# Kernel optimization log

Hardware: AMD Instinct MI355X
Metric: run time of the kernel (lower is better)

Reference implementation:

```python
import jax, jax.numpy as jnp
import numpy as np

N = 100000      # nodes
E = 1600000     # edges (avg degree 16)
ND = 64         # node feature dim (fiber degree-0 channels)
ED = 32         # edge feature dim
L = 3           # number of edge_update layers (num_layers - 1)
IN = ED + 2 * ND  # concat dim = 160
EPS = 1e-5
NEG_SLOPE = 0.01  # torch LeakyReLU default


def setup_inputs() -> dict:
    key = jax.random.key(0)
    ks = jax.random.split(key, 6)
    node_feat = jax.random.normal(ks[0], (N, ND), jnp.float32)
    edge_w = jax.random.normal(ks[1], (E, ED), jnp.float32)
    edge_i = jax.random.randint(ks[2], (E,), 0, N, jnp.int32)
    edge_j = jax.random.randint(ks[3], (E,), 0, N, jnp.int32)
    ln_g = jnp.ones((L, IN), jnp.float32)
    ln_b = jnp.zeros((L, IN), jnp.float32)
    w1 = jax.random.normal(ks[4], (L, IN, ED), jnp.float32) / np.sqrt(IN).astype(np.float32)
    b1 = jnp.zeros((L, ED), jnp.float32)
    w2 = jax.random.normal(ks[5], (L, ED, ED), jnp.float32) / np.sqrt(ED).astype(np.float32)
    b2 = jnp.zeros((L, ED), jnp.float32)
    return {"node_feat": node_feat, "edge_w": edge_w, "ln_g": ln_g, "ln_b": ln_b,
            "w1": w1, "b1": b1, "w2": w2, "b2": b2,
            "edge_i": edge_i, "edge_j": edge_j}


def _edge_update(nf, e, g, b, W1, B1, W2, B2, i, j):
    # gather per-edge endpoint features, concat with edge feature: [E, IN]
    x = jnp.concatenate([nf[i], nf[j], e], axis=-1)
    # LayerNorm over last dim
    mu = jnp.mean(x, axis=-1, keepdims=True)
    var = jnp.var(x, axis=-1, keepdims=True)
    x = (x - mu) * jax.lax.rsqrt(var + EPS) * g + b
    # Linear -> LeakyReLU -> Linear
    x = x @ W1 + B1
    x = jnp.where(x > 0, x, NEG_SLOPE * x)
    x = x @ W2 + B2
    return e + x  # residual edge update


def reference(node_feat, edge_w, ln_g, ln_b, w1, b1, w2, b2, edge_i, edge_j):
    e = edge_w
    for l in range(ln_g.shape[0]):  # small fixed layer count
        e = _edge_update(node_feat, e, ln_g[l], ln_b[l], w1[l], b1[l], w2[l], b2[l], edge_i, edge_j)
    return e
```

## Files before the change

### kernel.cpp

```cpp
#include <hip/hip_runtime.h>

#define EE     1600000
#define NN     100000
#define NDIM   64
#define EDIM   32
#define NLAYER 3
#define INDIM  160
#define TPB    256
#define EPT    2
#define EPB    (TPB*EPT)

static_assert(EE % EPB == 0, "grid must divide evenly");

__global__ __launch_bounds__(TPB) void node_precompute(
  const float* __restrict__ nf,  const float* __restrict__ lng,
  const float* __restrict__ lnb, const float* __restrict__ w1,
  const float* __restrict__ b1,
  float* __restrict__ P, float* __restrict__ nstat, float* __restrict__ cvec)
{
  __shared__ float sW[NLAYER*128*EDIM];
  __shared__ float sG[NLAYER*128];
  const int tid = threadIdx.x;

  #pragma unroll
  for (int it = 0; it < 12; ++it){
    const int c = tid + it*TPB;
    const int l = c >> 10, rem = c & 1023;
    const int d = rem >> 3, ks = (rem & 7) * 4;
    float4 v = *(const float4*)(w1 + (size_t)l*INDIM*EDIM + d*EDIM + ks);
    float* dst = &sW[l*128*EDIM + d*EDIM + ks];
    dst[0]=v.x; dst[1]=v.y; dst[2]=v.z; dst[3]=v.w;
  }
  if (tid < 96){
    const int l = tid >> 5, ks = (tid & 31) * 4;
    float4 v = *(const float4*)(lng + l*INDIM + ks);
    float* dst = &sG[l*128 + ks];
    dst[0]=v.x; dst[1]=v.y; dst[2]=v.z; dst[3]=v.w;
  }
  __syncthreads();

  if (blockIdx.x == 0 && tid < 96){
    const int l = tid >> 5, k = tid & 31;
    const float* wl = w1 + (size_t)l*INDIM*EDIM;
    float c2 = 0.f, c1 = b1[l*EDIM + k];
    for (int d = 0; d < INDIM; ++d){
      const float w = wl[d*EDIM + k];
      c2 = fmaf(lng[l*INDIM + d], w, c2);
      c1 = fmaf(lnb[l*INDIM + d], w, c1);
    }
    cvec[l*EDIM + k]      = c2;
    cvec[96 + l*EDIM + k] = c1;
  }

  const int n = blockIdx.x*TPB + tid;
  if (n >= NN) return;
  const float4* px = (const float4*)(nf + (size_t)n * NDIM);

  {
    float s = 0.f, q = 0.f;
    #pragma unroll 1
    for (int c = 0; c < 16; ++c){
      float4 v = px[c];
      s += v.x + v.y + v.z + v.w;
      q = fmaf(v.x,v.x,q); q = fmaf(v.y,v.y,q);
      q = fmaf(v.z,v.z,q); q = fmaf(v.w,v.w,q);
    }
    nstat[2*n] = s; nstat[2*n+1] = q;
  }

  #pragma unroll 1
  for (int lp = 0; lp < NLAYER*2; ++lp){
    const int l = lp >> 1, part = lp & 1;
    float acc[EDIM];
    #pragma unroll
    for (int k = 0; k < EDIM; ++k) acc[k] = 0.f;
    const float* wbl = &sW[(l*128 + part*64) * EDIM];
    const float* gbl = &sG[l*128 + part*64];
    #pragma unroll 1
    for (int c = 0; c < 16; ++c){
      float4 xv = px[c];
      const float xs[4] = {xv.x, xv.y, xv.z, xv.w};
      const int d0 = 4*c;
      #pragma unroll
      for (int u = 0; u < 4; ++u){
        const float xd = xs[u] * gbl[d0 + u];
        const float4* row = (const float4*)&wbl[(size_t)(d0+u)*EDIM];
        #pragma unroll
        for (int q8 = 0; q8 < 8; ++q8){
          float4 w = row[q8];
          acc[4*q8+0] = fmaf(xd, w.x, acc[4*q8+0]);
          acc[4*q8+1] = fmaf(xd, w.y, acc[4*q8+1]);
          acc[4*q8+2] = fmaf(xd, w.z, acc[4*q8+2]);
          acc[4*q8+3] = fmaf(xd, w.w, acc[4*q8+3]);
        }
      }
    }
    float* dst = P + ((size_t)l*NN + n)*64 + part*EDIM;
    #pragma unroll
    for (int q8 = 0; q8 < 8; ++q8)
      ((float4*)dst)[q8] = make_float4(acc[4*q8+0], acc[4*q8+1], acc[4*q8+2], acc[4*q8+3]);
  }
}

__global__ __launch_bounds__(TPB, 2) void edge_mlp_pre(
  const float* __restrict__ ew, const float* __restrict__ lng,
  const float* __restrict__ w1, const float* __restrict__ w2,
  const float* __restrict__ b2,
  const int* __restrict__ ei, const int* __restrict__ ej,
  const float* __restrict__ P, const float* __restrict__ nstat,
  const float* __restrict__ cvec, float* __restrict__ out)
{
  __shared__ float sW1E[NLAYER*EDIM*EDIM];
  __shared__ float sW2 [NLAYER*EDIM*EDIM];
  __shared__ float sGE [NLAYER*EDIM];
  __shared__ float sC2 [NLAYER*EDIM], sC1b[NLAYER*EDIM], sB2v[NLAYER*EDIM];

  const int tid = threadIdx.x;
  #pragma unroll
  for (int it = 0; it < 3; ++it){
    const int c = tid + it*TPB;
    const int l = c >> 8, rem = c & 255;
    const int d = rem >> 3, ks = (rem & 7) * 4;
    float4 v = *(const float4*)(w1 + (size_t)l*INDIM*EDIM + (size_t)(128+d)*EDIM + ks);
    float* dst = &sW1E[l*EDIM*EDIM + d*EDIM + ks];
    dst[0]=v.x; dst[1]=v.y; dst[2]=v.z; dst[3]=v.w;
  }
  #pragma unroll
  for (int it = 0; it < 3; ++it){
    const int c = tid + it*TPB;
    float4 v = ((const float4*)w2)[c];
    float* dst = &sW2[4*c];
    dst[0]=v.x; dst[1]=v.y; dst[2]=v.z; dst[3]=v.w;
  }
  if (tid < 96){
    sGE [tid] = lng[(tid>>5)*INDIM + 128 + (tid&31)];
    sB2v[tid] = b2[tid];
    sC2 [tid] = cvec[tid];
    sC1b[tid] = cvec[96 + tid];
  }
  __syncthreads();

  const int id0 = blockIdx.x * EPB + tid;
  const int id1 = id0 + TPB;
  const int i0 = ei[id0], j0 = ej[id0];
  const int i1 = ei[id1], j1 = ej[id1];

  const float2 sti0 = *(const float2*)(nstat + 2*(size_t)i0);
  const float2 stj0 = *(const float2*)(nstat + 2*(size_t)j0);
  const float2 sti1 = *(const float2*)(nstat + 2*(size_t)i1);
  const float2 stj1 = *(const float2*)(nstat + 2*(size_t)j1);
  const float sn0 = sti0.x + stj0.x, qn0 = sti0.y + stj0.y;
  const float sn1 = sti1.x + stj1.x, qn1 = sti1.y + stj1.y;

  float e0[EDIM], e1[EDIM];
  {
    const float4* a = (const float4*)(ew + (size_t)id0 * EDIM);
    const float4* b = (const float4*)(ew + (size_t)id1 * EDIM);
    #pragma unroll
    for (int c = 0; c < 8; ++c){
      float4 v = a[c];
      e0[4*c+0]=v.x; e0[4*c+1]=v.y; e0[4*c+2]=v.z; e0[4*c+3]=v.w;
      float4 u = b[c];
      e1[4*c+0]=u.x; e1[4*c+1]=u.y; e1[4*c+2]=u.z; e1[4*c+3]=u.w;
    }
  }

  #pragma unroll 1
  for (int l = 0; l < NLAYER; ++l){
    const float* Pl = P + (size_t)l * NN * 64;
    const float4* a0v = (const float4*)(Pl + (size_t)i0*64);
    const float4* b0v = (const float4*)(Pl + (size_t)j0*64 + EDIM);
    const float4* a1v = (const float4*)(Pl + (size_t)i1*64);
    const float4* b1v = (const float4*)(Pl + (size_t)j1*64 + EDIM);

    float S0[EDIM], S1[EDIM];
    #pragma unroll
    for (int c = 0; c < 8; ++c){
      float4 u = a0v[c], v = b0v[c];
      S0[4*c+0]=u.x+v.x; S0[4*c+1]=u.y+v.y; S0[4*c+2]=u.z+v.z; S0[4*c+3]=u.w+v.w;
      float4 p = a1v[c], r = b1v[c];
      S1[4*c+0]=p.x+r.x; S1[4*c+1]=p.y+r.y; S1[4*c+2]=p.z+r.z; S1[4*c+3]=p.w+r.w;
    }

    float se0=0.f, qe0=0.f, se1=0.f, qe1=0.f;
    #pragma unroll
    for (int d = 0; d < EDIM; ++d){
      se0 += e0[d]; qe0 = fmaf(e0[d], e0[d], qe0);
      se1 += e1[d]; qe1 = fmaf(e1[d], e1[d], qe1);
    }
    const float mu0 = (sn0 + se0) * (1.f/INDIM);
    const float va0 = fmaxf(fmaf(-mu0, mu0, (qn0 + qe0) * (1.f/INDIM)), 0.f);
    const float rs0 = rsqrtf(va0 + 1e-5f);
    const float nm0 = -mu0 * rs0;
    const float mu1 = (sn1 + se1) * (1.f/INDIM);
    const float va1 = fmaxf(fmaf(-mu1, mu1, (qn1 + qe1) * (1.f/INDIM)), 0.f);
    const float rs1 = rsqrtf(va1 + 1e-5f);
    const float nm1 = -mu1 * rs1;

    const float* wE = &sW1E[l*EDIM*EDIM];
    const float* gE = &sGE[l*EDIM];
    #pragma unroll
    for (int d = 0; d < EDIM; ++d){
      const float xd0 = gE[d]*e0[d], xd1 = gE[d]*e1[d];
      const float4* row = (const float4*)&wE[d*EDIM];
      #pragma unroll
      for (int q = 0; q < 8; ++q){
        float4 w = row[q];
        S0[4*q+0]=fmaf(xd0,w.x,S0[4*q+0]); S1[4*q+0]=fmaf(xd1,w.x,S1[4*q+0]);
        S0[4*q+1]=fmaf(xd0,w.y,S0[4*q+1]); S1[4*q+1]=fmaf(xd1,w.y,S1[4*q+1]);
        S0[4*q+2]=fmaf(xd0,w.z,S0[4*q+2]); S1[4*q+2]=fmaf(xd1,w.z,S1[4*q+2]);
        S0[4*q+3]=fmaf(xd0,w.w,S0[4*q+3]); S1[4*q+3]=fmaf(xd1,w.w,S1[4*q+3]);
      }
    }

    const float* c2  = &sC2 [l*EDIM];
    const float* c1b = &sC1b[l*EDIM];
    const float* bb2 = &sB2v[l*EDIM];
    #pragma unroll
    for (int k = 0; k < EDIM; ++k){
      float a = fmaf(rs0, S0[k], fmaf(nm0, c2[k], c1b[k]));
      S0[k] = fmaxf(a, 0.01f*a);
      float b = fmaf(rs1, S1[k], fmaf(nm1, c2[k], c1b[k]));
      S1[k] = fmaxf(b, 0.01f*b);
    }
    #pragma unroll
    for (int k = 0; k < EDIM; ++k){ e0[k] += bb2[k]; e1[k] += bb2[k]; }

    const float* w2l = &sW2[l*EDIM*EDIM];
    #pragma unroll
    for (int d = 0; d < EDIM; ++d){
      const float a = S0[d], b = S1[d];
      const float4* row = (const float4*)&w2l[d*EDIM];
      #pragma unroll
      for (int q = 0; q < 8; ++q){
        float4 w = row[q];
        e0[4*q+0]=fmaf(a,w.x,e0[4*q+0]); e1[4*q+0]=fmaf(b,w.x,e1[4*q+0]);
        e0[4*q+1]=fmaf(a,w.y,e0[4*q+1]); e1[4*q+1]=fmaf(b,w.y,e1[4*q+1]);
        e0[4*q+2]=fmaf(a,w.z,e0[4*q+2]); e1[4*q+2]=fmaf(b,w.z,e1[4*q+2]);
        e0[4*q+3]=fmaf(a,w.w,e0[4*q+3]); e1[4*q+3]=fmaf(b,w.w,e1[4*q+3]);
      }
    }
  }

  float4* o0 = (float4*)(out + (size_t)id0 * EDIM);
  float4* o1 = (float4*)(out + (size_t)id1 * EDIM);
  #pragma unroll
  for (int c = 0; c < 8; ++c){
    o0[c] = make_float4(e0[4*c+0], e0[4*c+1], e0[4*c+2], e0[4*c+3]);
    o1[c] = make_float4(e1[4*c+0], e1[4*c+1], e1[4*c+2], e1[4*c+3]);
  }
}

__global__ __launch_bounds__(TPB, 2) void edge_mlp_fused(
  const float* __restrict__ nf,  const float* __restrict__ ew,
  const float* __restrict__ lng, const float* __restrict__ lnb,
  const float* __restrict__ w1,  const float* __restrict__ b1,
  const float* __restrict__ w2,  const float* __restrict__ b2,
  const int* __restrict__ ei, const int* __restrict__ ej,
  float* __restrict__ out)
{
  __shared__ float sW1[INDIM*EDIM];
  __shared__ float sW2[EDIM*EDIM];
  __shared__ float sC2[EDIM], sC1b[EDIM], sB2[EDIM];

  const int tid = threadIdx.x;
  const int id0 = blockIdx.x * EPB + tid;
  const int id1 = id0 + TPB;

  const float4* pi0 = (const float4*)(nf + (size_t)ei[id0] * NDIM);
  const float4* pj0 = (const float4*)(nf + (size_t)ej[id0] * NDIM);
  const float4* pi1 = (const float4*)(nf + (size_t)ei[id1] * NDIM);
  const float4* pj1 = (const float4*)(nf + (size_t)ej[id1] * NDIM);

  float e0[EDIM], e1[EDIM];
  {
    const float4* a = (const float4*)(ew + (size_t)id0 * EDIM);
    const float4* b = (const float4*)(ew + (size_t)id1 * EDIM);
    #pragma unroll
    for (int c = 0; c < 8; ++c){
      float4 v = a[c];
      e0[4*c+0]=v.x; e0[4*c+1]=v.y; e0[4*c+2]=v.z; e0[4*c+3]=v.w;
      float4 u = b[c];
      e1[4*c+0]=u.x; e1[4*c+1]=u.y; e1[4*c+2]=u.z; e1[4*c+3]=u.w;
    }
  }

  #pragma unroll 1
  for (int l = 0; l < NLAYER; ++l){
    __syncthreads();
    const float* w1l = w1 + (size_t)l * INDIM * EDIM;

    #pragma unroll
    for (int it = 0; it < 5; ++it){
      const int c = tid + it * TPB;
      const int d = c >> 3, ks = (c & 7) * 4;
      float4 v = *(const float4*)(w1l + d * EDIM + ks);
      const float g = lng[l * INDIM + d];
      sW1[d*EDIM+ks+0] = g*v.x; sW1[d*EDIM+ks+1] = g*v.y;
      sW1[d*EDIM+ks+2] = g*v.z; sW1[d*EDIM+ks+3] = g*v.w;
    }
    {
      const int d = tid >> 3, ks = (tid & 7) * 4;
      float4 v = *(const float4*)(w2 + (size_t)l*EDIM*EDIM + d*EDIM + ks);
      sW2[d*EDIM+ks+0] = v.x; sW2[d*EDIM+ks+1] = v.y;
      sW2[d*EDIM+ks+2] = v.z; sW2[d*EDIM+ks+3] = v.w;
    }
    if (tid < EDIM){
      float c1 = b1[l*EDIM + tid];
      for (int d = 0; d < INDIM; ++d)
        c1 = fmaf(lnb[l*INDIM + d], w1l[d*EDIM + tid], c1);
      sC1b[tid] = c1;
      sB2[tid]  = b2[l*EDIM + tid];
    }
    __syncthreads();
    if (tid < EDIM){
      float s = 0.f;
      for (int d = 0; d < INDIM; ++d) s += sW1[d*EDIM + tid];
      sC2[tid] = s;
    }
    __syncthreads();

    float S0[EDIM], S1[EDIM];
    #pragma unroll
    for (int k = 0; k < EDIM; ++k){ S0[k] = 0.f; S1[k] = 0.f; }
    float sum0 = 0.f, sq0 = 0.f, sum1 = 0.f, sq1 = 0.f;

    auto dot_row = [&](float xv0, float xv1, const float4* row){
      sum0 += xv0; sq0 = fmaf(xv0, xv0, sq0);
      sum1 += xv1; sq1 = fmaf(xv1, xv1, sq1);
      #pragma unroll
      for (int q = 0; q < 8; ++q){
        float4 w = row[q];
        S0[4*q+0] = fmaf(xv0, w.x, S0[4*q+0]); S1[4*q+0] = fmaf(xv1, w.x, S1[4*q+0]);
        S0[4*q+1] = fmaf(xv0, w.y, S0[4*q+1]); S1[4*q+1] = fmaf(xv1, w.y, S1[4*q+1]);
        S0[4*q+2] = fmaf(xv0, w.z, S0[4*q+2]); S1[4*q+2] = fmaf(xv1, w.z, S1[4*q+2]);
        S0[4*q+3] = fmaf(xv0, w.w, S0[4*q+3]); S1[4*q+3] = fmaf(xv1, w.w, S1[4*q+3]);
      }
    };

    #pragma unroll 1
    for (int c = 0; c < 32; ++c){
      const float4 x0 = (c < 16) ? pi0[c] : pj0[c - 16];
      const float4 x1 = (c < 16) ? pi1[c] : pj1[c - 16];
      const float4* wr = (const float4*)&sW1[c * 4 * EDIM];
      dot_row(x0.x, x1.x, wr + 0);
      dot_row(x0.y, x1.y, wr + 8);
      dot_row(x0.z, x1.z, wr + 16);
      dot_row(x0.w, x1.w, wr + 24);
    }
    #pragma unroll
    for (int d = 0; d < EDIM; ++d){
      const float4* row = (const float4*)&sW1[(2*NDIM + d) * EDIM];
      dot_row(e0[d], e1[d], row);
    }

    const float mu0 = sum0 * (1.f/INDIM);
    const float va0 = fmaxf(fmaf(-mu0, mu0, sq0 * (1.f/INDIM)), 0.f);
    const float rs0 = rsqrtf(va0 + 1e-5f);
    const float nm0 = -mu0 * rs0;
    const float mu1 = sum1 * (1.f/INDIM);
    const float va1 = fmaxf(fmaf(-mu1, mu1, sq1 * (1.f/INDIM)), 0.f);
    const float rs1 = rsqrtf(va1 + 1e-5f);
    const float nm1 = -mu1 * rs1;

    float h0[EDIM], h1v[EDIM];
    #pragma unroll
    for (int k = 0; k < EDIM; ++k){
      float a = fmaf(rs0, S0[k], fmaf(nm0, sC2[k], sC1b[k]));
      h0[k]  = fmaxf(a, 0.01f * a);
      float b = fmaf(rs1, S1[k], fmaf(nm1, sC2[k], sC1b[k]));
      h1v[k] = fmaxf(b, 0.01f * b);
    }
    #pragma unroll
    for (int k = 0; k < EDIM; ++k){ e0[k] += sB2[k]; e1[k] += sB2[k]; }
    #pragma unroll
    for (int d = 0; d < EDIM; ++d){
      const float a = h0[d], b = h1v[d];
      const float4* row = (const float4*)&sW2[d * EDIM];
      #pragma unroll
      for (int q = 0; q < 8; ++q){
        float4 w = row[q];
        e0[4*q+0] = fmaf(a, w.x, e0[4*q+0]); e1[4*q+0] = fmaf(b, w.x, e1[4*q+0]);
        e0[4*q+1] = fmaf(a, w.y, e0[4*q+1]); e1[4*q+1] = fmaf(b, w.y, e1[4*q+1]);
        e0[4*q+2] = fmaf(a, w.z, e0[4*q+2]); e1[4*q+2] = fmaf(b, w.z, e1[4*q+2]);
        e0[4*q+3] = fmaf(a, w.w, e0[4*q+3]); e1[4*q+3] = fmaf(b, w.w, e1[4*q+3]);
      }
    }
  }

  float4* o0 = (float4*)(out + (size_t)id0 * EDIM);
  float4* o1 = (float4*)(out + (size_t)id1 * EDIM);
  #pragma unroll
  for (int c = 0; c < 8; ++c){
    o0[c] = make_float4(e0[4*c+0], e0[4*c+1], e0[4*c+2], e0[4*c+3]);
    o1[c] = make_float4(e1[4*c+0], e1[4*c+1], e1[4*c+2], e1[4*c+3]);
  }
}

extern "C" void kernel_launch(void* const* d_in, const int* in_sizes, int n_in,
                              void* d_out, int out_size, void* d_ws, size_t ws_size,
                              hipStream_t stream)
{
  const float* nf  = (const float*)d_in[0];
  const float* ew  = (const float*)d_in[1];
  const float* lng = (const float*)d_in[2];
  const float* lnb = (const float*)d_in[3];
  const float* w1  = (const float*)d_in[4];
  const float* b1  = (const float*)d_in[5];
  const float* w2  = (const float*)d_in[6];
  const float* b2  = (const float*)d_in[7];
  const int*   ei  = (const int*)d_in[8];
  const int*   ej  = (const int*)d_in[9];
  float* out = (float*)d_out;

  const size_t PBYTES = (size_t)NLAYER * NN * 64 * sizeof(float);
  const size_t SBYTES = (size_t)NN * 2 * sizeof(float);
  const size_t CBYTES = (size_t)2 * NLAYER * EDIM * sizeof(float);

  if (d_ws && ws_size >= PBYTES + SBYTES + CBYTES){
    float* P     = (float*)d_ws;
    float* nstat = (float*)((char*)d_ws + PBYTES);
    float* cvec  = (float*)((char*)d_ws + PBYTES + SBYTES);
    hipLaunchKernelGGL(node_precompute, dim3((NN + TPB - 1)/TPB), dim3(TPB), 0, stream,
                       nf, lng, lnb, w1, b1, P, nstat, cvec);
    hipLaunchKernelGGL(edge_mlp_pre, dim3(EE / EPB), dim3(TPB), 0, stream,
                       ew, lng, w1, w2, b2, ei, ej, P, nstat, cvec, out);
  } else {
    dim3 grid(EE / EPB), block(TPB);
    hipLaunchKernelGGL(edge_mlp_fused, grid, block, 0, stream,
                       nf, ew, lng, lnb, w1, b1, w2, b2, ei, ej, out);
  }
}
```

Before: 1.113 ms.

## Split node precompute across layer-parts grid and use one edge per thread

```diff
diff --git a/kernel.cpp b/kernel.cpp
--- a/kernel.cpp
+++ b/kernel.cpp
@@ -7,10 +7,8 @@
 #define NLAYER 3
 #define INDIM  160
 #define TPB    256
-#define EPT    2
-#define EPB    (TPB*EPT)
-
-static_assert(EE % EPB == 0, "grid must divide evenly");
+
+static_assert(EE % TPB == 0, "grid must divide evenly");
 
 __global__ __launch_bounds__(TPB) void node_precompute(
   const float* __restrict__ nf,  const float* __restrict__ lng,
@@ -18,45 +16,44 @@
   const float* __restrict__ b1,
   float* __restrict__ P, float* __restrict__ nstat, float* __restrict__ cvec)
 {
-  __shared__ float sW[NLAYER*128*EDIM];
-  __shared__ float sG[NLAYER*128];
-  const int tid = threadIdx.x;
-
-  #pragma unroll
-  for (int it = 0; it < 12; ++it){
+  __shared__ float sW[64*EDIM];
+  __shared__ float sG[64];
+  const int tid  = threadIdx.x;
+  const int lp   = blockIdx.y;
+  const int l    = lp >> 1, part = lp & 1;
+
+  #pragma unroll
+  for (int it = 0; it < 2; ++it){
     const int c = tid + it*TPB;
-    const int l = c >> 10, rem = c & 1023;
-    const int d = rem >> 3, ks = (rem & 7) * 4;
-    float4 v = *(const float4*)(w1 + (size_t)l*INDIM*EDIM + d*EDIM + ks);
-    float* dst = &sW[l*128*EDIM + d*EDIM + ks];
+    const int d = c >> 3, ks = (c & 7) * 4;
+    float4 v = *(const float4*)(w1 + (size_t)l*INDIM*EDIM + (size_t)(part*64 + d)*EDIM + ks);
+    float* dst = &sW[d*EDIM + ks];
     dst[0]=v.x; dst[1]=v.y; dst[2]=v.z; dst[3]=v.w;
   }
-  if (tid < 96){
-    const int l = tid >> 5, ks = (tid & 31) * 4;
-    float4 v = *(const float4*)(lng + l*INDIM + ks);
-    float* dst = &sG[l*128 + ks];
-    dst[0]=v.x; dst[1]=v.y; dst[2]=v.z; dst[3]=v.w;
+  if (tid < 16){
+    float4 v = *(const float4*)(lng + l*INDIM + part*64 + tid*4);
+    sG[4*tid+0]=v.x; sG[4*tid+1]=v.y; sG[4*tid+2]=v.z; sG[4*tid+3]=v.w;
   }
   __syncthreads();
 
-  if (blockIdx.x == 0 && tid < 96){
-    const int l = tid >> 5, k = tid & 31;
-    const float* wl = w1 + (size_t)l*INDIM*EDIM;
-    float c2 = 0.f, c1 = b1[l*EDIM + k];
+  if (lp == 0 && blockIdx.x == 0 && tid < 96){
+    const int ll = tid >> 5, k = tid & 31;
+    const float* wl = w1 + (size_t)ll*INDIM*EDIM;
+    float c2 = 0.f, c1 = b1[ll*EDIM + k];
     for (int d = 0; d < INDIM; ++d){
       const float w = wl[d*EDIM + k];
-      c2 = fmaf(lng[l*INDIM + d], w, c2);
-      c1 = fmaf(lnb[l*INDIM + d], w, c1);
-    }
-    cvec[l*EDIM + k]      = c2;
-    cvec[96 + l*EDIM + k] = c1;
+      c2 = fmaf(lng[ll*INDIM + d], w, c2);
+      c1 = fmaf(lnb[ll*INDIM + d], w, c1);
+    }
+    cvec[ll*EDIM + k]      = c2;
+    cvec[96 + ll*EDIM + k] = c1;
   }
 
   const int n = blockIdx.x*TPB + tid;
   if (n >= NN) return;
   const float4* px = (const float4*)(nf + (size_t)n * NDIM);
 
-  {
+  if (lp == 0){
     float s = 0.f, q = 0.f;
     #pragma unroll 1
     for (int c = 0; c < 16; ++c){
@@ -68,41 +65,35 @@
     nstat[2*n] = s; nstat[2*n+1] = q;
   }
 
+  float acc[EDIM];
+  #pragma unroll
+  for (int k = 0; k < EDIM; ++k) acc[k] = 0.f;
   #pragma unroll 1
-  for (int lp = 0; lp < NLAYER*2; ++lp){
-    const int l = lp >> 1, part = lp & 1;
-    float acc[EDIM];
-    #pragma unroll
-    for (int k = 0; k < EDIM; ++k) acc[k] = 0.f;
-    const float* wbl = &sW[(l*128 + part*64) * EDIM];
-    const float* gbl = &sG[l*128 + part*64];
-    #pragma unroll 1
-    for (int c = 0; c < 16; ++c){
-      float4 xv = px[c];
-      const float xs[4] = {xv.x, xv.y, xv.z, xv.w};
-      const int d0 = 4*c;
+  for (int c = 0; c < 16; ++c){
+    float4 xv = px[c];
+    const float xs[4] = {xv.x, xv.y, xv.z, xv.w};
+    const int d0 = 4*c;
+    #pragma unroll
+    for (int u = 0; u < 4; ++u){
+      const float xd = xs[u] * sG[d0 + u];
+      const float4* row = (const float4*)&sW[(size_t)(d0+u)*EDIM];
       #pragma unroll
-      for (int u = 0; u < 4; ++u){
-        const float xd = xs[u] * gbl[d0 + u];
-        const float4* row = (const float4*)&wbl[(size_t)(d0+u)*EDIM];
-        #pragma unroll
-        for (int q8 = 0; q8 < 8; ++q8){
-          float4 w = row[q8];
-          acc[4*q8+0] = fmaf(xd, w.x, acc[4*q8+0]);
-          acc[4*q8+1] = fmaf(xd, w.y, acc[4*q8+1]);
-          acc[4*q8+2] = fmaf(xd, w.z, acc[4*q8+2]);
-          acc[4*q8+3] = fmaf(xd, w.w, acc[4*q8+3]);
-        }
+      for (int q8 = 0; q8 < 8; ++q8){
+        float4 w = row[q8];
+        acc[4*q8+0] = fmaf(xd, w.x, acc[4*q8+0]);
+        acc[4*q8+1] = fmaf(xd, w.y, acc[4*q8+1]);
+        acc[4*q8+2] = fmaf(xd, w.z, acc[4*q8+2]);
+        acc[4*q8+3] = fmaf(xd, w.w, acc[4*q8+3]);
       }
     }
-    float* dst = P + ((size_t)l*NN + n)*64 + part*EDIM;
-    #pragma unroll
-    for (int q8 = 0; q8 < 8; ++q8)
-      ((float4*)dst)[q8] = make_float4(acc[4*q8+0], acc[4*q8+1], acc[4*q8+2], acc[4*q8+3]);
-  }
+  }
+  float* dst = P + ((size_t)l*NN + n)*64 + part*EDIM;
+  #pragma unroll
+  for (int q8 = 0; q8 < 8; ++q8)
+    ((float4*)dst)[q8] = make_float4(acc[4*q8+0], acc[4*q8+1], acc[4*q8+2], acc[4*q8+3]);
 }
 
-__global__ __launch_bounds__(TPB, 2) void edge_mlp_pre(
+__global__ __launch_bounds__(TPB, 4) void edge_mlp_pre(
   const float* __restrict__ ew, const float* __restrict__ lng,
   const float* __restrict__ w1, const float* __restrict__ w2,
   const float* __restrict__ b2,
@@ -140,76 +131,59 @@
   }
   __syncthreads();
 
-  const int id0 = blockIdx.x * EPB + tid;
-  const int id1 = id0 + TPB;
-  const int i0 = ei[id0], j0 = ej[id0];
-  const int i1 = ei[id1], j1 = ej[id1];
-
-  const float2 sti0 = *(const float2*)(nstat + 2*(size_t)i0);
-  const float2 stj0 = *(const float2*)(nstat + 2*(size_t)j0);
-  const float2 sti1 = *(const float2*)(nstat + 2*(size_t)i1);
-  const float2 stj1 = *(const float2*)(nstat + 2*(size_t)j1);
-  const float sn0 = sti0.x + stj0.x, qn0 = sti0.y + stj0.y;
-  const float sn1 = sti1.x + stj1.x, qn1 = sti1.y + stj1.y;
-
-  float e0[EDIM], e1[EDIM];
+  const int id = blockIdx.x * TPB + tid;
+  const int i = ei[id], j = ej[id];
+
+  const float2 sti = *(const float2*)(nstat + 2*(size_t)i);
+  const float2 stj = *(const float2*)(nstat + 2*(size_t)j);
+  const float sn = sti.x + stj.x, qn = sti.y + stj.y;
+
+  float e[EDIM];
   {
-    const float4* a = (const float4*)(ew + (size_t)id0 * EDIM);
-    const float4* b = (const float4*)(ew + (size_t)id1 * EDIM);
+    const float4* a = (const float4*)(ew + (size_t)id * EDIM);
     #pragma unroll
     for (int c = 0; c < 8; ++c){
       float4 v = a[c];
-      e0[4*c+0]=v.x; e0[4*c+1]=v.y; e0[4*c+2]=v.z; e0[4*c+3]=v.w;
-      float4 u = b[c];
-      e1[4*c+0]=u.x; e1[4*c+1]=u.y; e1[4*c+2]=u.z; e1[4*c+3]=u.w;
+      e[4*c+0]=v.x; e[4*c+1]=v.y; e[4*c+2]=v.z; e[4*c+3]=v.w;
     }
   }
 
   #pragma unroll 1
   for (int l = 0; l < NLAYER; ++l){
     const float* Pl = P + (size_t)l * NN * 64;
-    const float4* a0v = (const float4*)(Pl + (size_t)i0*64);
-    const float4* b0v = (const float4*)(Pl + (size_t)j0*64 + EDIM);
-    const float4* a1v = (const float4*)(Pl + (size_t)i1*64);
-    const float4* b1v = (const float4*)(Pl + (size_t)j1*64 + EDIM);
-
-    float S0[EDIM], S1[EDIM];
+    const float4* av = (const float4*)(Pl + (size_t)i*64);
+    const float4* bv = (const float4*)(Pl + (size_t)j*64 + EDIM);
+
+    float S[EDIM];
     #pragma unroll
     for (int c = 0; c < 8; ++c){
-      float4 u = a0v[c], v = b0v[c];
-      S0[4*c+0]=u.x+v.x; S0[4*c+1]=u.y+v.y; S0[4*c+2]=u.z+v.z; S0[4*c+3]=u.w+v.w;
-      float4 p = a1v[c], r = b1v[c];
-      S1[4*c+0]=p.x+r.x; S1[4*c+1]=p.y+r.y; S1[4*c+2]=p.z+r.z; S1[4*c+3]=p.w+r.w;
-    }
-
-    float se0=0.f, qe0=0.f, se1=0.f, qe1=0.f;
+      float4 u = av[c], v = bv[c];
+      S[4*c+0]=u.x+v.x; S[4*c+1]=u.y+v.y; S[4*c+2]=u.z+v.z; S[4*c+3]=u.w+v.w;
+    }
+
+    float se = 0.f, qe = 0.f;
     #pragma unroll
     for (int d = 0; d < EDIM; ++d){
-      se0 += e0[d]; qe0 = fmaf(e0[d], e0[d], qe0);
-      se1 += e1[d]; qe1 = fmaf(e1[d], e1[d], qe1);
-    }
-    const float mu0 = (sn0 + se0) * (1.f/INDIM);
-    const float va0 = fmaxf(fmaf(-mu0, mu0, (qn0 + qe0) * (1.f/INDIM)), 0.f);
-    const float rs0 = rsqrtf(va0 + 1e-5f);
-    const float nm0 = -mu0 * rs0;
-    const float mu1 = (sn1 + se1) * (1.f/INDIM);
-    const float va1 = fmaxf(fmaf(-mu1, mu1, (qn1 + qe1) * (1.f/INDIM)), 0.f);
-    const float rs1 = rsqrtf(va1 + 1e-5f);
-    const float nm1 = -mu1 * rs1;
+      se += e[d]; qe = fmaf(e[d], e[d], qe);
+    }
+    const float mu = (sn + se) * (1.f/INDIM);
+    const float va = fmaxf(fmaf(-mu, mu, (qn + qe) * (1.f/INDIM)), 0.f);
+    const float rs = rsqrtf(va + 1e-5f);
+    const float nm = -mu * rs;
 
     const float* wE = &sW1E[l*EDIM*EDIM];
     const float* gE = &sGE[l*EDIM];
     #pragma unroll
     for (int d = 0; d < EDIM; ++d){
-      const float xd0 = gE[d]*e0[d], xd1 = gE[d]*e1[d];
+      const float xd = gE[d]*e[d];
       const float4* row = (const float4*)&wE[d*EDIM];
       #pragma unroll
       for (int q = 0; q < 8; ++q){
         float4 w = row[q];
-        S0[4*q+0]=fmaf(xd0,w.x,S0[4*q+0]); S1[4*q+0]=fmaf(xd1,w.x,S1[4*q+0]);
-        S0[4*q+1]=fmaf(xd0,w.y,S0[4*q+1]); S1[4*q+1]=fmaf(xd1,w.y,S1[4*q+1]);
-        S0[4*q+2]=fmaf(xd0,w.z,S0[4*q+2]); S1[4*q+2]=fmaf(xd1,w.z,S1[4*q+2]);
-        S0[4*q+3]=fmaf(xd0,w.w,S0[4*q+3]); S1[4*q+3]=fmaf(xd1,w.w,S1[4*q+3]);
+        S[4*q+0]=fmaf(xd,w.x,S[4*q+0]);
+        S[4*q+1]=fmaf(xd,w.y,S[4*q+1]);
+        S[4*q+2]=fmaf(xd,w.z,S[4*q+2]);
+        S[4*q+3]=fmaf(xd,w.w,S[4*q+3]);
       }
     }
 
@@ -218,38 +192,37 @@
     const float* bb2 = &sB2v[l*EDIM];
     #pragma unroll
     for (int k = 0; k < EDIM; ++k){
-      float a = fmaf(rs0, S0[k], fmaf(nm0, c2[k], c1b[k]));
-      S0[k] = fmaxf(a, 0.01f*a);
-      float b = fmaf(rs1, S1[k], fmaf(nm1, c2[k], c1b[k]));
-      S1[k] = fmaxf(b, 0.01f*b);
-    }
-    #pragma unroll
-    for (int k = 0; k < EDIM; ++k){ e0[k] += bb2[k]; e1[k] += bb2[k]; }
+      float a = fmaf(rs, S[k], fmaf(nm, c2[k], c1b[k]));
+      S[k] = fmaxf(a, 0.01f*a);
+    }
+    #pragma unroll
+    for (int k = 0; k < EDIM; ++k) e[k] += bb2[k];
 
     const float* w2l = &sW2[l*EDIM*EDIM];
     #pragma unroll
     for (int d = 0; d < EDIM; ++d){
-      const float a = S0[d], b = S1[d];
+      const float a = S[d];
       const float4* row = (const float4*)&w2l[d*EDIM];
       #pragma unroll
       for (int q = 0; q < 8; ++q){
         float4 w = row[q];
-        e0[4*q+0]=fmaf(a,w.x,e0[4*q+0]); e1[4*q+0]=fmaf(b,w.x,e1[4*q+0]);
-        e0[4*q+1]=fmaf(a,w.y,e0[4*q+1]); e1[4*q+1]=fmaf(b,w.y,e1[4*q+1]);
-        e0[4*q+2]=fmaf(a,w.z,e0[4*q+2]); e1[4*q+2]=fmaf(b,w.z,e1[4*q+2]);
-        e0[4*q+3]=fmaf(a,w.w,e0[4*q+3]); e1[4*q+3]=fmaf(b,w.w,e1[4*q+3]);
+        e[4*q+0]=fmaf(a,w.x,e[4*q+0]);
+        e[4*q+1]=fmaf(a,w.y,e[4*q+1]);
+        e[4*q+2]=fmaf(a,w.z,e[4*q+2]);
+        e[4*q+3]=fmaf(a,w.w,e[4*q+3]);
       }
     }
   }
 
-  float4* o0 = (float4*)(out + (size_t)id0 * EDIM);
-  float4* o1 = (float4*)(out + (size_t)id1 * EDIM);
-  #pragma unroll
-  for (int c = 0; c < 8; ++c){
-    o0[c] = make_float4(e0[4*c+0], e0[4*c+1], e0[4*c+2], e0[4*c+3]);
-    o1[c] = make_float4(e1[4*c+0], e1[4*c+1], e1[4*c+2], e1[4*c+3]);
-  }
+  float4* o = (float4*)(out + (size_t)id * EDIM);
+  #pragma unroll
+  for (int c = 0; c < 8; ++c)
+    o[c] = make_float4(e[4*c+0], e[4*c+1], e[4*c+2], e[4*c+3]);
 }
+
+#define EPT    2
+#define EPB    (TPB*EPT)
+static_assert(EE % EPB == 0, "grid must divide evenly");
 
 __global__ __launch_bounds__(TPB, 2) void edge_mlp_fused(
   const float* __restrict__ nf,  const float* __restrict__ ew,
@@ -421,9 +394,10 @@
     float* P     = (float*)d_ws;
     float* nstat = (float*)((char*)d_ws + PBYTES);
     float* cvec  = (float*)((char*)d_ws + PBYTES + SBYTES);
-    hipLaunchKernelGGL(node_precompute, dim3((NN + TPB - 1)/TPB), dim3(TPB), 0, stream,
+    hipLaunchKernelGGL(node_precompute,
+                       dim3((NN + TPB - 1)/TPB, 6), dim3(TPB), 0, stream,
                        nf, lng, lnb, w1, b1, P, nstat, cvec);
-    hipLaunchKernelGGL(edge_mlp_pre, dim3(EE / EPB), dim3(TPB), 0, stream,
+    hipLaunchKernelGGL(edge_mlp_pre, dim3(EE / TPB), dim3(TPB), 0, stream,
                        ew, lng, w1, w2, b2, ei, ej, P, nstat, cvec, out);
   } else {
     dim3 grid(EE / EPB), block(TPB);
```

Result: faster. 898.9 us (-19.2%).
